# Performance work log

Measured on AMD Instinct MI355X. Metric: run time of the kernel, lower is better.

Reference implementation:

```python
import jax, jax.numpy as jnp
import numpy as np

N, E, D, L, RBF = 20000, 320000, 128, 3, 64
CUTOFF = 5.0
LN_EPS = 1e-5


def setup_inputs() -> dict:
    key = jax.random.key(0)
    ks = jax.random.split(key, 20)
    s = 0.05
    inp = {
        'z': jax.random.normal(ks[0], (N, 64), jnp.float32),
        'pos': jax.random.normal(ks[1], (N, 3), jnp.float32),
        'edge_index': jax.random.randint(ks[2], (2, E), 0, N),
        'in_w': jax.random.normal(ks[3], (64, D), jnp.float32) * s,
        'in_b': jnp.zeros((D,), jnp.float32),
        'filt_w': jax.random.normal(ks[4], (RBF, 3 * D), jnp.float32) * s,
        'filt_b': jnp.zeros((3 * D,), jnp.float32),
        'inter_w1': jax.random.normal(ks[5], (L, D, D), jnp.float32) * s,
        'inter_b1': jnp.zeros((L, D), jnp.float32),
        'inter_w2': jax.random.normal(ks[6], (L, D, 3 * D), jnp.float32) * s,
        'inter_b2': jnp.zeros((L, 3 * D), jnp.float32),
        'mix_mu_w': jax.random.normal(ks[7], (L, D, 2 * D), jnp.float32) * s,
        'mix_w1': jax.random.normal(ks[8], (L, 2 * D, D), jnp.float32) * s,
        'mix_b1': jnp.zeros((L, D), jnp.float32),
        'mix_w2': jax.random.normal(ks[9], (L, D, 3 * D), jnp.float32) * s,
        'mix_b2': jnp.zeros((L, 3 * D), jnp.float32),
        'mu_proj_w': jnp.zeros((D,), jnp.float32),  # nn.init.constant_(0.0) in source
        'ln_g': jnp.ones((D,), jnp.float32),
        'ln_b': jnp.zeros((D,), jnp.float32),
    }
    return inp


def painn_forward(z, pos, in_w, in_b, filt_w, filt_b, inter_w1, inter_b1,
                  inter_w2, inter_b2, mix_mu_w, mix_w1, mix_b1, mix_w2, mix_b2,
                  mu_proj_w, ln_g, ln_b, edge_index):
    idx_i, idx_j = edge_index[0], edge_index[1]
    # edge geometry
    r_ij = pos[idx_j] - pos[idx_i]                               # [E,3]
    d_ij = jnp.maximum(jnp.linalg.norm(r_ij, axis=1, keepdims=True), 1e-8)  # [E,1]
    dir_ij = r_ij / d_ij                                          # [E,3]
    # gaussian smearing
    offset = jnp.linspace(0.0, CUTOFF, RBF).astype(jnp.float32)
    coeff = -0.5 / (offset[1] - offset[0]) ** 2
    phi = jnp.exp(coeff * (d_ij - offset) ** 2)                   # [E,RBF]
    # cosine cutoff
    xc = jnp.clip(d_ij / CUTOFF, 0.0, 1.0)
    fcut = 0.5 * (jnp.cos(jnp.pi * xc) + 1.0) * (xc < 1.0)        # [E,1]
    filters = (phi @ filt_w + filt_b) * fcut                      # [E,3D]
    filters = jnp.clip(jnp.nan_to_num(filters), -5.0, 5.0)
    Wij = filters[:, None, :]                                     # [E,1,3D]

    q = jax.nn.silu(z @ in_w + in_b)[:, None, :]                  # [N,1,D]
    mu = jnp.zeros((N, 3, D), q.dtype)                            # [N,3,D]

    for l in range(L):
        # interaction (edge gather -> gate -> scatter-add)
        x = jax.nn.silu(q @ inter_w1[l] + inter_b1[l]) @ inter_w2[l] + inter_b2[l]  # [N,1,3D]
        xj = x[idx_j] * Wij                                       # [E,1,3D]
        dq, dmuR, dmumu = jnp.split(xj, 3, axis=-1)               # each [E,1,D]
        muj = mu[idx_j]                                           # [E,3,D]
        q = q + jax.ops.segment_sum(dq, idx_i, num_segments=N)
        dmu = dmuR * dir_ij[:, :, None] + dmumu * muj             # [E,3,D]
        mu = mu + jax.ops.segment_sum(dmu, idx_i, num_segments=N)
        # intra-atomic mixing
        mu_mix = mu @ mix_mu_w[l]                                  # [N,3,2D]
        mu_V, mu_W = jnp.split(mu_mix, 2, axis=-1)                 # [N,3,D]
        mu_Vn = jnp.sqrt(jnp.sum(mu_V ** 2, axis=-2, keepdims=True) + 1e-8)  # [N,1,D]
        ctx = jnp.concatenate([q, mu_Vn], axis=-1)                 # [N,1,2D]
        xm = jax.nn.silu(ctx @ mix_w1[l] + mix_b1[l]) @ mix_w2[l] + mix_b2[l]  # [N,1,3D]
        dq_i, dmu_i, dqmu_i = jnp.split(xm, 3, axis=-1)
        q = q + dq_i + dqmu_i * jnp.sum(mu_V * mu_W, axis=1, keepdims=True)
        mu = mu + dmu_i * mu_W

    node_attr = jnp.clip(jnp.nan_to_num(q[:, 0, :]), -5.0, 5.0)   # [N,D]
    mean = jnp.mean(node_attr, axis=-1, keepdims=True)
    var = jnp.var(node_attr, axis=-1, keepdims=True)
    node_attr = (node_attr - mean) * jax.lax.rsqrt(var + LN_EPS) * ln_g + ln_b
    node_attr = jnp.nan_to_num(jnp.tanh(node_attr))

    mu = jnp.nan_to_num(mu)
    mu_node = jax.ops.segment_sum(mu[idx_j], idx_i, num_segments=N)  # [N,3,D]
    mu_node = jnp.clip(jnp.nan_to_num(mu_node), -5.0, 5.0)
    pos_attr = jnp.clip(jnp.nan_to_num(mu_node @ mu_proj_w), -5.0, 5.0)  # [N,3]
    return node_attr, pos_attr


def reference(z, pos, edge_index, in_w, in_b, filt_w, filt_b, inter_w1, inter_b1,
              inter_w2, inter_b2, mix_mu_w, mix_w1, mix_b1, mix_w2, mix_b2,
              mu_proj_w, ln_g, ln_b):
    return painn_forward(z, pos, in_w, in_b, filt_w, filt_b, inter_w1, inter_b1,
                         inter_w2, inter_b2, mix_mu_w, mix_w1, mix_b1, mix_w2,
                         mix_b2, mu_proj_w, ln_g, ln_b, edge_index)
```

## Files before the change

kernel.cpp:

```cpp
#include <hip/hip_runtime.h>
#include <math.h>

#ifndef M_PI
#define M_PI 3.14159265358979323846
#endif

static constexpr int N_NODES = 20000;
static constexpr int N_EDGES = 320000;
static constexpr int NLAYER  = 3;
static constexpr int NB_SCAN = (N_NODES + 255) / 256;
static constexpr int TAB_T   = 1024;

typedef _Float16 f16;
typedef __attribute__((ext_vector_type(2))) _Float16 f16x2;
typedef __attribute__((ext_vector_type(8))) _Float16 f16x8;
typedef __attribute__((ext_vector_type(4))) float f32x4;

__device__ __forceinline__ void storev(float* p, float v) { *p = v; }
__device__ __forceinline__ void storev(f16* p, float v)   { *p = (f16)v; }

__global__ void k_hist(const int* __restrict__ idx_i, int* __restrict__ cnt) {
  int e = blockIdx.x * 256 + threadIdx.x;
  if (e < N_EDGES) atomicAdd(&cnt[idx_i[e]], 1);
}

__global__ void k_scan_blk(const int* __restrict__ cnt, int* __restrict__ incl,
                           int* __restrict__ bsum) {
  __shared__ int buf[256];
  int t = threadIdx.x;
  int i = blockIdx.x * 256 + t;
  int v = (i < N_NODES) ? cnt[i] : 0;
  buf[t] = v;
  __syncthreads();
  #pragma unroll
  for (int off = 1; off < 256; off <<= 1) {
    int x = (t >= off) ? buf[t - off] : 0;
    __syncthreads();
    buf[t] += x;
    __syncthreads();
  }
  if (i < N_NODES) incl[i] = buf[t];
  if (t == 255) bsum[blockIdx.x] = buf[255];
}

__global__ void k_scan_top(int* __restrict__ bsum) {
  __shared__ int buf[128];
  int t = threadIdx.x;
  int v = (t < NB_SCAN) ? bsum[t] : 0;
  buf[t] = v;
  __syncthreads();
  #pragma unroll
  for (int off = 1; off < 128; off <<= 1) {
    int x = (t >= off) ? buf[t - off] : 0;
    __syncthreads();
    buf[t] += x;
    __syncthreads();
  }
  if (t <= NB_SCAN) bsum[t] = buf[t] - v;
}

__global__ void k_scan_add(const int* __restrict__ cnt, const int* __restrict__ incl,
                           const int* __restrict__ bsum, int* __restrict__ rs,
                           int* __restrict__ cur) {
  int i = blockIdx.x * 256 + threadIdx.x;
  if (i < N_NODES) {
    int v = bsum[blockIdx.x] + incl[i] - cnt[i];
    rs[i] = v;
    cur[i] = v;
  }
  if (i == 0) rs[N_NODES] = bsum[NB_SCAN];
}

__global__ void k_fill_geom(const int* __restrict__ idx_all, const float* __restrict__ pos,
                            int* __restrict__ cur, float4* __restrict__ geo,
                            int* __restrict__ jperm) {
  int e = blockIdx.x * 256 + threadIdx.x;
  if (e >= N_EDGES) return;
  int i = idx_all[e];
  int j = idx_all[N_EDGES + e];
  int p = atomicAdd(&cur[i], 1);
  float rx = pos[j*3+0] - pos[i*3+0];
  float ry = pos[j*3+1] - pos[i*3+1];
  float rz = pos[j*3+2] - pos[i*3+2];
  float d = sqrtf(rx*rx + ry*ry + rz*rz);
  d = fmaxf(d, 1e-8f);
  float inv = 1.0f / d;
  geo[p] = make_float4(d, rx*inv, ry*inv, rz*inv);
  jperm[p] = j;
}

struct WJob { const float* src; f16* dst; int kshift; int ld; int col0; int nk; };
struct WJobs { WJob j[16]; };

__global__ __launch_bounds__(256) void k_prep(WJobs jb, const float* __restrict__ filt_w,
                                              const float* __restrict__ filt_b,
                                              f16* __restrict__ tab) {
  if (blockIdx.y < 16) {
    WJob w = jb.j[blockIdx.y];
    int t = blockIdx.x * 256 + threadIdx.x;
    if (t >= w.nk) return;
    int K = 1 << w.kshift;
    int n = t >> w.kshift;
    int k = t & (K - 1);
    w.dst[t] = (f16)w.src[(size_t)k * w.ld + w.col0 + n];
    return;
  }
  if (blockIdx.x >= 128) return;
  const int t = (blockIdx.y - 16) * 128 + blockIdx.x;
  __shared__ float ph[64];
  const int tid = threadIdx.x;
  const float dist = 5.0f * (float)t / (float)(TAB_T - 1);
  const float delta = 5.0f / 63.0f;
  const float coeff = -0.5f / (delta * delta);
  if (tid < 64) {
    float u = dist - delta * (float)tid;
    ph[tid] = expf(coeff * u * u);
  }
  __syncthreads();
  float xc = dist * 0.2f;
  float fc = (xc < 1.0f) ? 0.5f * (cosf((float)M_PI * xc) + 1.0f) : 0.0f;
  for (int n = tid; n < 384; n += 256) {
    float acc = 0.f;
    #pragma unroll
    for (int k = 0; k < 64; ++k) acc += ph[k] * filt_w[k * 384 + n];
    float v = (acc + filt_b[n]) * fc;
    v = fminf(fmaxf(v, -5.0f), 5.0f);
    tab[(size_t)t * 384 + n] = (f16)v;
  }
}

template<int EPI, typename AT, typename CT>
__global__ __launch_bounds__(256) void k_mgemm(
    const AT* __restrict__ A, const f16* __restrict__ Wt,
    const float* __restrict__ bias, CT* __restrict__ C,
    int M, int K, int ldc) {
  __shared__ f16 As[128 * 32];
  __shared__ f16 Bs[128 * 32];
  const int bm = blockIdx.x * 128;
  const int bn = blockIdx.y * 128;
  const int tid = threadIdx.x;
  const int wave = tid >> 6, lane = tid & 63;
  const int wm = (wave & 1) * 64, wn = (wave >> 1) * 64;
  const int lr = lane & 15;
  const int lk = lane >> 4;
  const int srow = tid >> 1;
  const int sc0 = (tid & 1) * 2;
  const int sw = (srow >> 1) & 3;
  f32x4 acc[4][4] = {};
  for (int k0 = 0; k0 < K; k0 += 32) {
    {
      int gm = bm + srow;
      f16x8 c0, c1;
      if (gm < M) {
        if constexpr (sizeof(AT) == 2) {
          const f16* ap = (const f16*)A + (size_t)gm * K + k0 + sc0 * 8;
          c0 = *(const f16x8*)ap;
          c1 = *(const f16x8*)(ap + 8);
        } else {
          const float* ap = (const float*)A + (size_t)gm * K + k0 + sc0 * 8;
          float4 v0 = ((const float4*)ap)[0];
          float4 v1 = ((const float4*)ap)[1];
          float4 v2 = ((const float4*)ap)[2];
          float4 v3 = ((const float4*)ap)[3];
          c0[0]=(f16)v0.x; c0[1]=(f16)v0.y; c0[2]=(f16)v0.z; c0[3]=(f16)v0.w;
          c0[4]=(f16)v1.x; c0[5]=(f16)v1.y; c0[6]=(f16)v1.z; c0[7]=(f16)v1.w;
          c1[0]=(f16)v2.x; c1[1]=(f16)v2.y; c1[2]=(f16)v2.z; c1[3]=(f16)v2.w;
          c1[4]=(f16)v3.x; c1[5]=(f16)v3.y; c1[6]=(f16)v3.z; c1[7]=(f16)v3.w;
        }
      } else {
        #pragma unroll
        for (int u = 0; u < 8; ++u) { c0[u] = (f16)0.f; c1[u] = (f16)0.f; }
      }
      *(f16x8*)&As[srow * 32 + ((sc0 ^ sw) << 3)]       = c0;
      *(f16x8*)&As[srow * 32 + (((sc0 + 1) ^ sw) << 3)] = c1;
    }
    {
      const f16* bp = Wt + (size_t)(bn + srow) * K + k0 + sc0 * 8;
      f16x8 b0 = *(const f16x8*)bp;
      f16x8 b1 = *(const f16x8*)(bp + 8);
      *(f16x8*)&Bs[srow * 32 + ((sc0 ^ sw) << 3)]       = b0;
      *(f16x8*)&Bs[srow * 32 + (((sc0 + 1) ^ sw) << 3)] = b1;
    }
    __syncthreads();
    f16x8 af[4], bf[4];
    #pragma unroll
    for (int mt = 0; mt < 4; ++mt) {
      int r = wm + mt * 16 + lr;
      af[mt] = *(const f16x8*)&As[r * 32 + ((lk ^ ((r >> 1) & 3)) << 3)];
    }
    #pragma unroll
    for (int nt = 0; nt < 4; ++nt) {
      int r = wn + nt * 16 + lr;
      bf[nt] = *(const f16x8*)&Bs[r * 32 + ((lk ^ ((r >> 1) & 3)) << 3)];
    }
    #pragma unroll
    for (int mt = 0; mt < 4; ++mt)
      #pragma unroll
      for (int nt = 0; nt < 4; ++nt)
        acc[mt][nt] = __builtin_amdgcn_mfma_f32_16x16x32_f16(af[mt], bf[nt], acc[mt][nt], 0, 0, 0);
    __syncthreads();
  }
  #pragma unroll
  for (int mt = 0; mt < 4; ++mt) {
    int gm0 = bm + wm + mt * 16 + lk * 4;
    #pragma unroll
    for (int nt = 0; nt < 4; ++nt) {
      int gn = bn + wn + nt * 16 + lr;
      float bv = bias ? bias[gn] : 0.0f;
      #pragma unroll
      for (int rr = 0; rr < 4; ++rr) {
        int gm = gm0 + rr;
        if (gm >= M) continue;
        float v = acc[mt][nt][rr] + bv;
        if (EPI == 1) v = v / (1.0f + expf(-v));
        storev(&C[(size_t)gm * ldc + gn], v);
      }
    }
  }
}

__global__ __launch_bounds__(256) void k_fused_i(
    const float* __restrict__ q, const f16* __restrict__ W1, const float* __restrict__ b1,
    const f16* __restrict__ W2, const float* __restrict__ b2,
    f16* __restrict__ xout, int M) {
  __shared__ f16 As[64 * 32];
  __shared__ f16 Hs[64 * 132];
  const int tid = threadIdx.x;
  const int wave = tid >> 6, lane = tid & 63;
  const int wm = (wave & 1) * 32, wn = (wave >> 1) * 64;
  const int lr = lane & 15, lk = lane >> 4;
  const int srow = tid >> 2, c8 = tid & 3;
  const int sw = (srow >> 1) & 3;
  const int bm = blockIdx.x * 64;
  f32x4 acc[2][4] = {};
  for (int k0 = 0; k0 < 128; k0 += 32) {
    {
      int gm = bm + srow;
      f16x8 c0;
      if (gm < M) {
        const float* ap = q + (size_t)gm * 128 + k0 + c8 * 8;
        float4 v0 = ((const float4*)ap)[0];
        float4 v1 = ((const float4*)ap)[1];
        c0[0]=(f16)v0.x; c0[1]=(f16)v0.y; c0[2]=(f16)v0.z; c0[3]=(f16)v0.w;
        c0[4]=(f16)v1.x; c0[5]=(f16)v1.y; c0[6]=(f16)v1.z; c0[7]=(f16)v1.w;
      } else {
        #pragma unroll
        for (int u = 0; u < 8; ++u) c0[u] = (f16)0.f;
      }
      *(f16x8*)&As[srow * 32 + ((c8 ^ sw) << 3)] = c0;
    }
    __syncthreads();
    f16x8 af[2], bf[4];
    #pragma unroll
    for (int mt = 0; mt < 2; ++mt) {
      int r = wm + mt * 16 + lr;
      af[mt] = *(const f16x8*)&As[r * 32 + ((lk ^ ((r >> 1) & 3)) << 3)];
    }
    #pragma unroll
    for (int nt = 0; nt < 4; ++nt)
      bf[nt] = *(const f16x8*)&W1[(size_t)(wn + nt * 16 + lr) * 128 + k0 + lk * 8];
    #pragma unroll
    for (int mt = 0; mt < 2; ++mt)
      #pragma unroll
      for (int nt = 0; nt < 4; ++nt)
        acc[mt][nt] = __builtin_amdgcn_mfma_f32_16x16x32_f16(af[mt], bf[nt], acc[mt][nt], 0, 0, 0);
    __syncthreads();
  }
  #pragma unroll
  for (int mt = 0; mt < 2; ++mt)
    #pragma unroll
    for (int nt = 0; nt < 4; ++nt) {
      int col = wn + nt * 16 + lr;
      float bv = b1[col];
      #pragma unroll
      for (int rr = 0; rr < 4; ++rr) {
        int row = wm + mt * 16 + lk * 4 + rr;
        float v = acc[mt][nt][rr] + bv;
        v = v / (1.0f + expf(-v));
        Hs[row * 132 + col] = (f16)v;
      }
    }
  __syncthreads();
  #pragma unroll
  for (int cc = 0; cc < 3; ++cc) {
    f32x4 a2[2][4] = {};
    for (int k0 = 0; k0 < 128; k0 += 32) {
      f16x8 af2[2], bf2[4];
      #pragma unroll
      for (int mt = 0; mt < 2; ++mt)
        af2[mt] = *(const f16x8*)&Hs[(wm + mt * 16 + lr) * 132 + k0 + lk * 8];
      #pragma unroll
      for (int nt = 0; nt < 4; ++nt)
        bf2[nt] = *(const f16x8*)&W2[(size_t)(cc * 128 + wn + nt * 16 + lr) * 128 + k0 + lk * 8];
      #pragma unroll
      for (int mt = 0; mt < 2; ++mt)
        #pragma unroll
        for (int nt = 0; nt < 4; ++nt)
          a2[mt][nt] = __builtin_amdgcn_mfma_f32_16x16x32_f16(af2[mt], bf2[nt], a2[mt][nt], 0, 0, 0);
    }
    #pragma unroll
    for (int mt = 0; mt < 2; ++mt)
      #pragma unroll
      for (int nt = 0; nt < 4; ++nt) {
        int gn = cc * 128 + wn + nt * 16 + lr;
        float bv = b2[gn];
        #pragma unroll
        for (int rr = 0; rr < 4; ++rr) {
          int gm = bm + wm + mt * 16 + lk * 4 + rr;
          if (gm >= M) continue;
          xout[(size_t)gm * 384 + gn] = (f16)(a2[mt][nt][rr] + bv);
        }
      }
  }
}

__global__ __launch_bounds__(256) void k_fused_mx(
    float* __restrict__ q, f16* __restrict__ mu,
    const f16* __restrict__ Wmu,
    const f16* __restrict__ W1, const float* __restrict__ b1,
    const f16* __restrict__ W2, const float* __restrict__ b2) {
  __shared__ __align__(16) char pool[50688 + 24576];
  f16* MM  = (f16*)pool;
  f16* As4 = (f16*)(pool + 50688);
  f16* VN  = (f16*)(pool + 50688);
  f16* HS  = (f16*)(pool + 50688 + 8192);

  const int tid = threadIdx.x;
  const int wave = tid >> 6, lane = tid & 63;
  const int lr = lane & 15, lk = lane >> 4;
  const int n0 = blockIdx.x * 32;
  const int r0 = n0 * 3;

  #pragma unroll
  for (int rep = 0; rep < 6; ++rep) {
    int idx = rep * 256 + tid;
    int row = idx >> 4;
    int g   = idx & 15;
    int kb = g >> 2, c8 = g & 3;
    f16x8 v = *(const f16x8*)(mu + (size_t)(r0 + row) * 128 + g * 8);
    *(f16x8*)&As4[((kb * 96 + row) << 5) + (((c8 ^ ((row >> 1) & 3))) << 3)] = v;
  }
  __syncthreads();

  const int wmA = (wave & 1) * 48;
  const int wnA0 = (wave >> 1) * 64;
  #pragma unroll
  for (int half = 0; half < 2; ++half) {
    f32x4 accA[3][4] = {};
    #pragma unroll
    for (int kk = 0; kk < 4; ++kk) {
      f16x8 af[3], bf[4];
      #pragma unroll
      for (int mt = 0; mt < 3; ++mt) {
        int r = wmA + mt * 16 + lr;
        af[mt] = *(const f16x8*)&As4[((kk * 96 + r) << 5) + ((lk ^ ((r >> 1) & 3)) << 3)];
      }
      #pragma unroll
      for (int nt = 0; nt < 4; ++nt)
        bf[nt] = *(const f16x8*)&Wmu[(size_t)(half * 128 + wnA0 + nt * 16 + lr) * 128 + kk * 32 + lk * 8];
      #pragma unroll
      for (int mt = 0; mt < 3; ++mt)
        #pragma unroll
        for (int nt = 0; nt < 4; ++nt)
          accA[mt][nt] = __builtin_amdgcn_mfma_f32_16x16x32_f16(af[mt], bf[nt], accA[mt][nt], 0, 0, 0);
    }
    #pragma unroll
    for (int mt = 0; mt < 3; ++mt)
      #pragma unroll
      for (int nt = 0; nt < 4; ++nt) {
        int col = half * 128 + wnA0 + nt * 16 + lr;
        #pragma unroll
        for (int rr = 0; rr < 4; ++rr) {
          int row = wmA + mt * 16 + lk * 4 + rr;
          MM[row * 264 + col] = (f16)accA[mt][nt][rr];
        }
      }
  }
  __syncthreads();

  #pragma unroll
  for (int rep = 0; rep < 16; ++rep) {
    int idx = rep * 256 + tid;
    int nn = idx >> 7, c = idx & 127;
    float V0 = (float)MM[(nn * 3 + 0) * 264 + c];
    float V1 = (float)MM[(nn * 3 + 1) * 264 + c];
    float V2 = (float)MM[(nn * 3 + 2) * 264 + c];
    float vnv = sqrtf(V0 * V0 + V1 * V1 + V2 * V2 + 1e-8f);
    int kb = c >> 5, c8 = (c >> 3) & 3, ce = c & 7;
    VN[((kb * 32 + nn) << 5) + ((c8 ^ ((nn >> 1) & 3)) << 3) + ce] = (f16)vnv;
  }
  __syncthreads();

  const int wmB = (wave & 1) * 16, wnB = (wave >> 1) * 64;
  f32x4 accB[4] = {};
  #pragma unroll
  for (int kk = 0; kk < 8; ++kk) {
    f16x8 af;
    int row = wmB + lr;
    if (kk < 4) {
      const float* qp_ = q + (size_t)(n0 + row) * 128 + kk * 32 + lk * 8;
      float4 v0 = ((const float4*)qp_)[0];
      float4 v1 = ((const float4*)qp_)[1];
      af[0]=(f16)v0.x; af[1]=(f16)v0.y; af[2]=(f16)v0.z; af[3]=(f16)v0.w;
      af[4]=(f16)v1.x; af[5]=(f16)v1.y; af[6]=(f16)v1.z; af[7]=(f16)v1.w;
    } else {
      af = *(const f16x8*)&VN[(((kk - 4) * 32 + row) << 5) + ((lk ^ ((row >> 1) & 3)) << 3)];
    }
    f16x8 bf[4];
    #pragma unroll
    for (int nt = 0; nt < 4; ++nt)
      bf[nt] = *(const f16x8*)&W1[(size_t)(wnB + nt * 16 + lr) * 256 + kk * 32 + lk * 8];
    #pragma unroll
    for (int nt = 0; nt < 4; ++nt)
      accB[nt] = __builtin_amdgcn_mfma_f32_16x16x32_f16(af, bf[nt], accB[nt], 0, 0, 0);
  }
  #pragma unroll
  for (int nt = 0; nt < 4; ++nt) {
    int col = wnB + nt * 16 + lr;
    float bv = b1[col];
    #pragma unroll
    for (int rr = 0; rr < 4; ++rr) {
      int row = wmB + lk * 4 + rr;
      float v = accB[nt][rr] + bv;
      v = v / (1.0f + expf(-v));
      HS[row * 132 + col] = (f16)v;
    }
  }
  __syncthreads();

  f32x4 accC[3][4] = {};
  #pragma unroll
  for (int cc = 0; cc < 3; ++cc)
    #pragma unroll
    for (int kk = 0; kk < 4; ++kk) {
      f16x8 af = *(const f16x8*)&HS[(wmB + lr) * 132 + kk * 32 + lk * 8];
      f16x8 bf[4];
      #pragma unroll
      for (int nt = 0; nt < 4; ++nt)
        bf[nt] = *(const f16x8*)&W2[(size_t)(cc * 128 + wnB + nt * 16 + lr) * 128 + kk * 32 + lk * 8];
      #pragma unroll
      for (int nt = 0; nt < 4; ++nt)
        accC[cc][nt] = __builtin_amdgcn_mfma_f32_16x16x32_f16(af, bf[nt], accC[cc][nt], 0, 0, 0);
    }
  #pragma unroll
  for (int nt = 0; nt < 4; ++nt) {
    int col = wnB + nt * 16 + lr;
    float b_dq = b2[col], b_dmu = b2[128 + col], b_dqmu = b2[256 + col];
    #pragma unroll
    for (int rr = 0; rr < 4; ++rr) {
      int nn = wmB + lk * 4 + rr;
      int gm = n0 + nn;
      float dq   = accC[0][nt][rr] + b_dq;
      float dmu  = accC[1][nt][rr] + b_dmu;
      float dqmu = accC[2][nt][rr] + b_dqmu;
      float V0 = (float)MM[(nn * 3 + 0) * 264 + col], W0 = (float)MM[(nn * 3 + 0) * 264 + 128 + col];
      float V1 = (float)MM[(nn * 3 + 1) * 264 + col], W1v = (float)MM[(nn * 3 + 1) * 264 + 128 + col];
      float V2 = (float)MM[(nn * 3 + 2) * 264 + col], W2v = (float)MM[(nn * 3 + 2) * 264 + 128 + col];
      float svw = V0 * W0 + V1 * W1v + V2 * W2v;
      size_t qi = (size_t)gm * 128 + col;
      q[qi] += dq + dqmu * svw;
      f16* mr = mu + (size_t)gm * 384;
      mr[col]       = (f16)((float)mr[col]       + dmu * W0);
      mr[128 + col] = (f16)((float)mr[128 + col] + dmu * W1v);
      mr[256 + col] = (f16)((float)mr[256 + col] + dmu * W2v);
    }
  }
}

template<bool HASMU>
__global__ __launch_bounds__(256) void k_edge_msg(
    const int* __restrict__ rs, const int* __restrict__ jperm,
    const f16* __restrict__ x, const f16* __restrict__ tab,
    const float4* __restrict__ geo, const f16* __restrict__ mu_in,
    float* __restrict__ q, f16* __restrict__ mu_out) {
  const int wid  = threadIdx.x >> 6;
  const int lane = threadIdx.x & 63;
  const int i = blockIdx.x * 4 + wid;
  if (i >= N_NODES) return;
  const int d0 = lane * 2;
  const float scale = (float)(TAB_T - 1) / 5.0f;
  float aqx = 0.f, aqy = 0.f;
  float a0x = 0.f, a0y = 0.f, a1x = 0.f, a1y = 0.f, a2x = 0.f, a2y = 0.f;
  const int s = rs[i], e = rs[i + 1];

  for (int p = s; p < e; ++p) {
    int j = jperm[p];
    float4 g = geo[p];
    float u = fminf(g.x, 5.0f) * scale;
    int t0 = min((int)u, TAB_T - 2);
    float fr = u - (float)t0, fo = 1.0f - fr;
    const f16* ta = tab + (size_t)t0 * 384;
    const f16* xj = x + (size_t)j * 384;
    f16x2 ta0 = *(const f16x2*)(ta + d0);
    f16x2 ta1 = *(const f16x2*)(ta + 128 + d0);
    f16x2 tb0 = *(const f16x2*)(ta + 384 + d0);
    f16x2 tb1 = *(const f16x2*)(ta + 512 + d0);
    f16x2 xv0 = *(const f16x2*)(xj + d0);
    f16x2 xv1 = *(const f16x2*)(xj + 128 + d0);
    float W0x = fo * (float)ta0[0] + fr * (float)tb0[0];
    float W0y = fo * (float)ta0[1] + fr * (float)tb0[1];
    float W1x = fo * (float)ta1[0] + fr * (float)tb1[0];
    float W1y = fo * (float)ta1[1] + fr * (float)tb1[1];
    float m1x = (float)xv1[0] * W1x, m1y = (float)xv1[1] * W1y;
    aqx = fmaf((float)xv0[0], W0x, aqx);
    aqy = fmaf((float)xv0[1], W0y, aqy);
    if constexpr (HASMU) {
      f16x2 ta2 = *(const f16x2*)(ta + 256 + d0);
      f16x2 tb2 = *(const f16x2*)(ta + 640 + d0);
      f16x2 xv2 = *(const f16x2*)(xj + 256 + d0);
      const f16* mj = mu_in + (size_t)j * 384;
      f16x2 mv0 = *(const f16x2*)(mj + d0);
      f16x2 mv1 = *(const f16x2*)(mj + 128 + d0);
      f16x2 mv2 = *(const f16x2*)(mj + 256 + d0);
      float W2x = fo * (float)ta2[0] + fr * (float)tb2[0];
      float W2y = fo * (float)ta2[1] + fr * (float)tb2[1];
      float m2x = (float)xv2[0] * W2x, m2y = (float)xv2[1] * W2y;
      a0x += m1x * g.y + m2x * (float)mv0[0];
      a0y += m1y * g.y + m2y * (float)mv0[1];
      a1x += m1x * g.z + m2x * (float)mv1[0];
      a1y += m1y * g.z + m2y * (float)mv1[1];
      a2x += m1x * g.w + m2x * (float)mv2[0];
      a2y += m1y * g.w + m2y * (float)mv2[1];
    } else {
      a0x += m1x * g.y; a0y += m1y * g.y;
      a1x += m1x * g.z; a1y += m1y * g.z;
      a2x += m1x * g.w; a2y += m1y * g.w;
    }
  }

  float* qp = q + (size_t)i * 128 + d0;
  float2 qv = *(float2*)qp;
  qv.x += aqx; qv.y += aqy;
  *(float2*)qp = qv;
  f16* mout = mu_out + (size_t)i * 384;
  f16x2 o0, o1, o2;
  if constexpr (HASMU) {
    const f16* min_ = mu_in + (size_t)i * 384;
    f16x2 i0 = *(const f16x2*)(min_ + d0);
    f16x2 i1 = *(const f16x2*)(min_ + 128 + d0);
    f16x2 i2 = *(const f16x2*)(min_ + 256 + d0);
    o0[0] = (f16)((float)i0[0] + a0x); o0[1] = (f16)((float)i0[1] + a0y);
    o1[0] = (f16)((float)i1[0] + a1x); o1[1] = (f16)((float)i1[1] + a1y);
    o2[0] = (f16)((float)i2[0] + a2x); o2[1] = (f16)((float)i2[1] + a2y);
  } else {
    o0[0] = (f16)a0x; o0[1] = (f16)a0y;
    o1[0] = (f16)a1x; o1[1] = (f16)a1y;
    o2[0] = (f16)a2x; o2[1] = (f16)a2y;
  }
  *(f16x2*)(mout + d0)       = o0;
  *(f16x2*)(mout + 128 + d0) = o1;
  *(f16x2*)(mout + 256 + d0) = o2;
}

__global__ __launch_bounds__(256) void k_outputs(
    const int* __restrict__ rs, const int* __restrict__ jperm,
    const f16* __restrict__ mu, const float* __restrict__ w, float* __restrict__ pos_out,
    const float* __restrict__ q, const float* __restrict__ g_, const float* __restrict__ b_,
    float* __restrict__ out_node) {
  const int wid  = threadIdx.x >> 6;
  const int lane = threadIdx.x & 63;
  const int i = blockIdx.x * 4 + wid;
  if (i >= N_NODES) return;
  const int d0 = lane * 2;
  if (blockIdx.y == 1) {
    float2 v = *(const float2*)(q + (size_t)i * 128 + d0);
    float v0 = fminf(fmaxf(v.x, -5.f), 5.f);
    float v1 = fminf(fmaxf(v.y, -5.f), 5.f);
    float s = v0 + v1, s2 = v0 * v0 + v1 * v1;
    #pragma unroll
    for (int off = 32; off > 0; off >>= 1) {
      s  += __shfl_down(s,  off, 64);
      s2 += __shfl_down(s2, off, 64);
    }
    s  = __shfl(s,  0, 64);
    s2 = __shfl(s2, 0, 64);
    float mean = s * (1.0f / 128.0f);
    float var  = s2 * (1.0f / 128.0f) - mean * mean;
    float r = rsqrtf(var + 1e-5f);
    out_node[(size_t)i * 128 + d0]     = tanhf((v0 - mean) * r * g_[d0]     + b_[d0]);
    out_node[(size_t)i * 128 + d0 + 1] = tanhf((v1 - mean) * r * g_[d0 + 1] + b_[d0 + 1]);
    return;
  }
  float a0x = 0.f, a0y = 0.f, a1x = 0.f, a1y = 0.f, a2x = 0.f, a2y = 0.f;
  const int s = rs[i], e = rs[i + 1];
  int p = s;
  for (; p + 2 <= e; p += 2) {
    int jA = jperm[p], jB = jperm[p + 1];
    const f16* mA = mu + (size_t)jA * 384;
    const f16* mB = mu + (size_t)jB * 384;
    f16x2 A0 = *(const f16x2*)(mA + d0);
    f16x2 A1 = *(const f16x2*)(mA + 128 + d0);
    f16x2 A2 = *(const f16x2*)(mA + 256 + d0);
    f16x2 B0 = *(const f16x2*)(mB + d0);
    f16x2 B1 = *(const f16x2*)(mB + 128 + d0);
    f16x2 B2 = *(const f16x2*)(mB + 256 + d0);
    a0x += (float)A0[0] + (float)B0[0]; a0y += (float)A0[1] + (float)B0[1];
    a1x += (float)A1[0] + (float)B1[0]; a1y += (float)A1[1] + (float)B1[1];
    a2x += (float)A2[0] + (float)B2[0]; a2y += (float)A2[1] + (float)B2[1];
  }
  for (; p < e; ++p) {
    int j = jperm[p];
    const f16* mj = mu + (size_t)j * 384;
    f16x2 A0 = *(const f16x2*)(mj + d0);
    f16x2 A1 = *(const f16x2*)(mj + 128 + d0);
    f16x2 A2 = *(const f16x2*)(mj + 256 + d0);
    a0x += (float)A0[0]; a0y += (float)A0[1];
    a1x += (float)A1[0]; a1y += (float)A1[1];
    a2x += (float)A2[0]; a2y += (float)A2[1];
  }
  float wx = w[d0], wy = w[d0 + 1];
  float s0 = fminf(fmaxf(a0x, -5.f), 5.f) * wx + fminf(fmaxf(a0y, -5.f), 5.f) * wy;
  float s1 = fminf(fmaxf(a1x, -5.f), 5.f) * wx + fminf(fmaxf(a1y, -5.f), 5.f) * wy;
  float s2 = fminf(fmaxf(a2x, -5.f), 5.f) * wx + fminf(fmaxf(a2y, -5.f), 5.f) * wy;
  #pragma unroll
  for (int off = 32; off > 0; off >>= 1) {
    s0 += __shfl_down(s0, off, 64);
    s1 += __shfl_down(s1, off, 64);
    s2 += __shfl_down(s2, off, 64);
  }
  if (lane == 0) {
    pos_out[(size_t)i * 3 + 0] = fminf(fmaxf(s0, -5.f), 5.f);
    pos_out[(size_t)i * 3 + 1] = fminf(fmaxf(s1, -5.f), 5.f);
    pos_out[(size_t)i * 3 + 2] = fminf(fmaxf(s2, -5.f), 5.f);
  }
}

extern "C" void kernel_launch(void* const* d_in, const int* in_sizes, int n_in,
                              void* d_out, int out_size, void* d_ws, size_t ws_size,
                              hipStream_t stream) {
  const float* z         = (const float*)d_in[0];
  const float* pos       = (const float*)d_in[1];
  const int*   edge_idx  = (const int*)d_in[2];
  const float* in_w      = (const float*)d_in[3];
  const float* in_b      = (const float*)d_in[4];
  const float* filt_w    = (const float*)d_in[5];
  const float* filt_b    = (const float*)d_in[6];
  const float* inter_w1  = (const float*)d_in[7];
  const float* inter_b1  = (const float*)d_in[8];
  const float* inter_w2  = (const float*)d_in[9];
  const float* inter_b2  = (const float*)d_in[10];
  const float* mix_mu_w  = (const float*)d_in[11];
  const float* mix_w1    = (const float*)d_in[12];
  const float* mix_b1    = (const float*)d_in[13];
  const float* mix_w2    = (const float*)d_in[14];
  const float* mix_b2    = (const float*)d_in[15];
  const float* mu_proj_w = (const float*)d_in[16];
  const float* ln_g      = (const float*)d_in[17];
  const float* ln_b      = (const float*)d_in[18];

  char* base = (char*)d_ws;
  size_t off = 0;
  auto alloc = [&](size_t bytes) -> char* {
    char* p = base + off;
    off += (bytes + 255) & ~(size_t)255;
    return p;
  };
  float*  q     = (float*)alloc((size_t)N_NODES * 128 * 4);
  f16*    x16   = (f16*)alloc((size_t)N_NODES * 384 * 2);
  f16*    mu_a  = (f16*)alloc((size_t)N_NODES * 384 * 2);
  f16*    mu_b  = (f16*)alloc((size_t)N_NODES * 384 * 2);
  float4* geo   = (float4*)alloc((size_t)N_EDGES * 16);
  int*    cnt   = (int*)alloc((size_t)N_NODES * 4);
  int*    incl  = (int*)alloc((size_t)N_NODES * 4);
  int*    bsum  = (int*)alloc(128 * 4);
  int*    rs    = (int*)alloc((size_t)(N_NODES + 1) * 4);
  int*    cur   = (int*)alloc((size_t)N_NODES * 4);
  int*    jperm = (int*)alloc((size_t)N_EDGES * 4);
  f16*    tab   = (f16*)alloc((size_t)TAB_T * 384 * 2);
  f16* wt_in = (f16*)alloc((size_t)128 * 64 * 2);
  f16* wt_i1 = (f16*)alloc((size_t)3 * 128 * 128 * 2);
  f16* wt_i2 = (f16*)alloc((size_t)3 * 384 * 128 * 2);
  f16* wt_mu = (f16*)alloc((size_t)3 * 256 * 128 * 2);
  f16* wt_x1 = (f16*)alloc((size_t)3 * 128 * 256 * 2);
  f16* wt_x2 = (f16*)alloc((size_t)3 * 384 * 128 * 2);
  if (off > ws_size) return;

  float* out_node = (float*)d_out;
  float* out_pos  = (float*)d_out + (size_t)N_NODES * 128;

  {
    WJobs jb;
    int ji = 0;
    jb.j[ji++] = {in_w, wt_in, 6, 128, 0, 128 * 64};
    for (int l = 0; l < 3; ++l)
      jb.j[ji++] = {inter_w1 + (size_t)l*128*128, wt_i1 + (size_t)l*128*128, 7, 128, 0, 128*128};
    for (int l = 0; l < 3; ++l)
      jb.j[ji++] = {inter_w2 + (size_t)l*128*384, wt_i2 + (size_t)l*384*128, 7, 384, 0, 384*128};
    for (int l = 0; l < 3; ++l)
      jb.j[ji++] = {mix_mu_w + (size_t)l*128*256, wt_mu + (size_t)l*256*128, 7, 256, 0, 256*128};
    for (int l = 0; l < 3; ++l)
      jb.j[ji++] = {mix_w1 + (size_t)l*256*128, wt_x1 + (size_t)l*128*256, 8, 128, 0, 128*256};
    for (int l = 0; l < 3; ++l)
      jb.j[ji++] = {mix_w2 + (size_t)l*128*384, wt_x2 + (size_t)l*384*128, 7, 384, 0, 384*128};
    dim3 g(192, 24);
    k_prep<<<g, 256, 0, stream>>>(jb, filt_w, filt_b, tab);
  }

  hipMemsetAsync(cnt, 0, (size_t)N_NODES * 4, stream);
  k_hist<<<N_EDGES / 256, 256, 0, stream>>>(edge_idx, cnt);
  k_scan_blk<<<NB_SCAN, 256, 0, stream>>>(cnt, incl, bsum);
  k_scan_top<<<1, 128, 0, stream>>>(bsum);
  k_scan_add<<<NB_SCAN, 256, 0, stream>>>(cnt, incl, bsum, rs, cur);
  k_fill_geom<<<N_EDGES / 256, 256, 0, stream>>>(edge_idx, pos, cur, geo, jperm);

  dim3 ge((N_NODES + 127) / 128, 1);
  k_mgemm<1, float, float><<<ge, 256, 0, stream>>>(z, wt_in, in_b, q, N_NODES, 64, 128);

  f16* mu_cur = mu_a;
  f16* mu_nxt = mu_b;
  const int gn4 = (N_NODES + 3) / 4;
  const int gf  = (N_NODES + 63) / 64;
  const int gmx = N_NODES / 32;
  for (int l = 0; l < NLAYER; ++l) {
    k_fused_i<<<gf, 256, 0, stream>>>(q, wt_i1 + (size_t)l*128*128, inter_b1 + (size_t)l*128,
                                      wt_i2 + (size_t)l*384*128, inter_b2 + (size_t)l*384,
                                      x16, N_NODES);
    if (l == 0)
      k_edge_msg<false><<<gn4, 256, 0, stream>>>(rs, jperm, x16, tab, geo, mu_cur, q, mu_nxt);
    else
      k_edge_msg<true><<<gn4, 256, 0, stream>>>(rs, jperm, x16, tab, geo, mu_cur, q, mu_nxt);
    { f16* t = mu_cur; mu_cur = mu_nxt; mu_nxt = t; }
    k_fused_mx<<<gmx, 256, 0, stream>>>(q, mu_cur, wt_mu + (size_t)l*256*128,
                                        wt_x1 + (size_t)l*128*256, mix_b1 + (size_t)l*128,
                                        wt_x2 + (size_t)l*384*128, mix_b2 + (size_t)l*384);
  }

  dim3 go(gn4, 2);
  k_outputs<<<go, 256, 0, stream>>>(rs, jperm, mu_cur, mu_proj_w, out_pos,
                                    q, ln_g, ln_b, out_node);
}
```

Measured before the change: 587.3 us.

## Fuse interaction MLP into embedding and previous mix kernels; skip zero-weight gather

```diff
diff --git a/kernel.cpp b/kernel.cpp
--- a/kernel.cpp
+++ b/kernel.cpp
@@ -15,9 +15,6 @@
 typedef __attribute__((ext_vector_type(2))) _Float16 f16x2;
 typedef __attribute__((ext_vector_type(8))) _Float16 f16x8;
 typedef __attribute__((ext_vector_type(4))) float f32x4;
-
-__device__ __forceinline__ void storev(float* p, float v) { *p = v; }
-__device__ __forceinline__ void storev(f16* p, float v)   { *p = (f16)v; }
 
 __global__ void k_hist(const int* __restrict__ idx_i, int* __restrict__ cnt) {
   int e = blockIdx.x * 256 + threadIdx.x;
@@ -129,201 +126,125 @@
   }
 }
 
-template<int EPI, typename AT, typename CT>
-__global__ __launch_bounds__(256) void k_mgemm(
-    const AT* __restrict__ A, const f16* __restrict__ Wt,
-    const float* __restrict__ bias, CT* __restrict__ C,
-    int M, int K, int ldc) {
-  __shared__ f16 As[128 * 32];
-  __shared__ f16 Bs[128 * 32];
-  const int bm = blockIdx.x * 128;
-  const int bn = blockIdx.y * 128;
+__global__ __launch_bounds__(256) void k_embed_i(
+    const float* __restrict__ z, const f16* __restrict__ Win, const float* __restrict__ bin,
+    const f16* __restrict__ Wi1, const float* __restrict__ bi1,
+    const f16* __restrict__ Wi2, const float* __restrict__ bi2,
+    float* __restrict__ q, f16* __restrict__ xout) {
+  __shared__ __align__(16) char pool[16896];
+  f16* QS  = (f16*)pool;
+  f16* H2S = (f16*)(pool + 8448);
   const int tid = threadIdx.x;
   const int wave = tid >> 6, lane = tid & 63;
-  const int wm = (wave & 1) * 64, wn = (wave >> 1) * 64;
-  const int lr = lane & 15;
-  const int lk = lane >> 4;
-  const int srow = tid >> 1;
-  const int sc0 = (tid & 1) * 2;
-  const int sw = (srow >> 1) & 3;
-  f32x4 acc[4][4] = {};
-  for (int k0 = 0; k0 < K; k0 += 32) {
-    {
-      int gm = bm + srow;
-      f16x8 c0, c1;
-      if (gm < M) {
-        if constexpr (sizeof(AT) == 2) {
-          const f16* ap = (const f16*)A + (size_t)gm * K + k0 + sc0 * 8;
-          c0 = *(const f16x8*)ap;
-          c1 = *(const f16x8*)(ap + 8);
-        } else {
-          const float* ap = (const float*)A + (size_t)gm * K + k0 + sc0 * 8;
-          float4 v0 = ((const float4*)ap)[0];
-          float4 v1 = ((const float4*)ap)[1];
-          float4 v2 = ((const float4*)ap)[2];
-          float4 v3 = ((const float4*)ap)[3];
-          c0[0]=(f16)v0.x; c0[1]=(f16)v0.y; c0[2]=(f16)v0.z; c0[3]=(f16)v0.w;
-          c0[4]=(f16)v1.x; c0[5]=(f16)v1.y; c0[6]=(f16)v1.z; c0[7]=(f16)v1.w;
-          c1[0]=(f16)v2.x; c1[1]=(f16)v2.y; c1[2]=(f16)v2.z; c1[3]=(f16)v2.w;
-          c1[4]=(f16)v3.x; c1[5]=(f16)v3.y; c1[6]=(f16)v3.z; c1[7]=(f16)v3.w;
-        }
-      } else {
-        #pragma unroll
-        for (int u = 0; u < 8; ++u) { c0[u] = (f16)0.f; c1[u] = (f16)0.f; }
+  const int lr = lane & 15, lk = lane >> 4;
+  const int wmB = (wave & 1) * 16, wnB = (wave >> 1) * 64;
+  const int n0 = blockIdx.x * 32;
+
+  f32x4 accP[4] = {};
+  #pragma unroll
+  for (int kk = 0; kk < 2; ++kk) {
+    const float* zp = z + (size_t)(n0 + wmB + lr) * 64 + kk * 32 + lk * 8;
+    float4 v0 = ((const float4*)zp)[0];
+    float4 v1 = ((const float4*)zp)[1];
+    f16x8 af;
+    af[0]=(f16)v0.x; af[1]=(f16)v0.y; af[2]=(f16)v0.z; af[3]=(f16)v0.w;
+    af[4]=(f16)v1.x; af[5]=(f16)v1.y; af[6]=(f16)v1.z; af[7]=(f16)v1.w;
+    f16x8 bf[4];
+    #pragma unroll
+    for (int nt = 0; nt < 4; ++nt)
+      bf[nt] = *(const f16x8*)&Win[(size_t)(wnB + nt * 16 + lr) * 64 + kk * 32 + lk * 8];
+    #pragma unroll
+    for (int nt = 0; nt < 4; ++nt)
+      accP[nt] = __builtin_amdgcn_mfma_f32_16x16x32_f16(af, bf[nt], accP[nt], 0, 0, 0);
+  }
+  #pragma unroll
+  for (int nt = 0; nt < 4; ++nt) {
+    int col = wnB + nt * 16 + lr;
+    float bv = bin[col];
+    #pragma unroll
+    for (int rr = 0; rr < 4; ++rr) {
+      int row = wmB + lk * 4 + rr;
+      float v = accP[nt][rr] + bv;
+      v = v / (1.0f + expf(-v));
+      q[(size_t)(n0 + row) * 128 + col] = v;
+      QS[row * 132 + col] = (f16)v;
+    }
+  }
+  __syncthreads();
+
+  f32x4 accD[4] = {};
+  #pragma unroll
+  for (int kk = 0; kk < 4; ++kk) {
+    f16x8 af = *(const f16x8*)&QS[(wmB + lr) * 132 + kk * 32 + lk * 8];
+    f16x8 bf[4];
+    #pragma unroll
+    for (int nt = 0; nt < 4; ++nt)
+      bf[nt] = *(const f16x8*)&Wi1[(size_t)(wnB + nt * 16 + lr) * 128 + kk * 32 + lk * 8];
+    #pragma unroll
+    for (int nt = 0; nt < 4; ++nt)
+      accD[nt] = __builtin_amdgcn_mfma_f32_16x16x32_f16(af, bf[nt], accD[nt], 0, 0, 0);
+  }
+  #pragma unroll
+  for (int nt = 0; nt < 4; ++nt) {
+    int col = wnB + nt * 16 + lr;
+    float bv = bi1[col];
+    #pragma unroll
+    for (int rr = 0; rr < 4; ++rr) {
+      int row = wmB + lk * 4 + rr;
+      float v = accD[nt][rr] + bv;
+      v = v / (1.0f + expf(-v));
+      H2S[row * 132 + col] = (f16)v;
+    }
+  }
+  __syncthreads();
+
+  #pragma unroll
+  for (int cc = 0; cc < 3; ++cc) {
+    f32x4 accE[4] = {};
+    #pragma unroll
+    for (int kk = 0; kk < 4; ++kk) {
+      f16x8 af = *(const f16x8*)&H2S[(wmB + lr) * 132 + kk * 32 + lk * 8];
+      f16x8 bf[4];
+      #pragma unroll
+      for (int nt = 0; nt < 4; ++nt)
+        bf[nt] = *(const f16x8*)&Wi2[(size_t)(cc * 128 + wnB + nt * 16 + lr) * 128 + kk * 32 + lk * 8];
+      #pragma unroll
+      for (int nt = 0; nt < 4; ++nt)
+        accE[nt] = __builtin_amdgcn_mfma_f32_16x16x32_f16(af, bf[nt], accE[nt], 0, 0, 0);
+    }
+    #pragma unroll
+    for (int nt = 0; nt < 4; ++nt) {
+      int gn = cc * 128 + wnB + nt * 16 + lr;
+      float bv = bi2[gn];
+      #pragma unroll
+      for (int rr = 0; rr < 4; ++rr) {
+        int gm = n0 + wmB + lk * 4 + rr;
+        xout[(size_t)gm * 384 + gn] = (f16)(accE[nt][rr] + bv);
       }
-      *(f16x8*)&As[srow * 32 + ((sc0 ^ sw) << 3)]       = c0;
-      *(f16x8*)&As[srow * 32 + (((sc0 + 1) ^ sw) << 3)] = c1;
-    }
-    {
-      const f16* bp = Wt + (size_t)(bn + srow) * K + k0 + sc0 * 8;
-      f16x8 b0 = *(const f16x8*)bp;
-      f16x8 b1 = *(const f16x8*)(bp + 8);
-      *(f16x8*)&Bs[srow * 32 + ((sc0 ^ sw) << 3)]       = b0;
-      *(f16x8*)&Bs[srow * 32 + (((sc0 + 1) ^ sw) << 3)] = b1;
-    }
-    __syncthreads();
-    f16x8 af[4], bf[4];
-    #pragma unroll
-    for (int mt = 0; mt < 4; ++mt) {
-      int r = wm + mt * 16 + lr;
-      af[mt] = *(const f16x8*)&As[r * 32 + ((lk ^ ((r >> 1) & 3)) << 3)];
-    }
-    #pragma unroll
-    for (int nt = 0; nt < 4; ++nt) {
-      int r = wn + nt * 16 + lr;
-      bf[nt] = *(const f16x8*)&Bs[r * 32 + ((lk ^ ((r >> 1) & 3)) << 3)];
-    }
-    #pragma unroll
-    for (int mt = 0; mt < 4; ++mt)
-      #pragma unroll
-      for (int nt = 0; nt < 4; ++nt)
-        acc[mt][nt] = __builtin_amdgcn_mfma_f32_16x16x32_f16(af[mt], bf[nt], acc[mt][nt], 0, 0, 0);
-    __syncthreads();
-  }
-  #pragma unroll
-  for (int mt = 0; mt < 4; ++mt) {
-    int gm0 = bm + wm + mt * 16 + lk * 4;
-    #pragma unroll
-    for (int nt = 0; nt < 4; ++nt) {
-      int gn = bn + wn + nt * 16 + lr;
-      float bv = bias ? bias[gn] : 0.0f;
-      #pragma unroll
-      for (int rr = 0; rr < 4; ++rr) {
-        int gm = gm0 + rr;
-        if (gm >= M) continue;
-        float v = acc[mt][nt][rr] + bv;
-        if (EPI == 1) v = v / (1.0f + expf(-v));
-        storev(&C[(size_t)gm * ldc + gn], v);
-      }
-    }
-  }
-}
-
-__global__ __launch_bounds__(256) void k_fused_i(
-    const float* __restrict__ q, const f16* __restrict__ W1, const float* __restrict__ b1,
-    const f16* __restrict__ W2, const float* __restrict__ b2,
-    f16* __restrict__ xout, int M) {
-  __shared__ f16 As[64 * 32];
-  __shared__ f16 Hs[64 * 132];
-  const int tid = threadIdx.x;
-  const int wave = tid >> 6, lane = tid & 63;
-  const int wm = (wave & 1) * 32, wn = (wave >> 1) * 64;
-  const int lr = lane & 15, lk = lane >> 4;
-  const int srow = tid >> 2, c8 = tid & 3;
-  const int sw = (srow >> 1) & 3;
-  const int bm = blockIdx.x * 64;
-  f32x4 acc[2][4] = {};
-  for (int k0 = 0; k0 < 128; k0 += 32) {
-    {
-      int gm = bm + srow;
-      f16x8 c0;
-      if (gm < M) {
-        const float* ap = q + (size_t)gm * 128 + k0 + c8 * 8;
-        float4 v0 = ((const float4*)ap)[0];
-        float4 v1 = ((const float4*)ap)[1];
-        c0[0]=(f16)v0.x; c0[1]=(f16)v0.y; c0[2]=(f16)v0.z; c0[3]=(f16)v0.w;
-        c0[4]=(f16)v1.x; c0[5]=(f16)v1.y; c0[6]=(f16)v1.z; c0[7]=(f16)v1.w;
-      } else {
-        #pragma unroll
-        for (int u = 0; u < 8; ++u) c0[u] = (f16)0.f;
-      }
-      *(f16x8*)&As[srow * 32 + ((c8 ^ sw) << 3)] = c0;
-    }
-    __syncthreads();
-    f16x8 af[2], bf[4];
-    #pragma unroll
-    for (int mt = 0; mt < 2; ++mt) {
-      int r = wm + mt * 16 + lr;
-      af[mt] = *(const f16x8*)&As[r * 32 + ((lk ^ ((r >> 1) & 3)) << 3)];
-    }
-    #pragma unroll
-    for (int nt = 0; nt < 4; ++nt)
-      bf[nt] = *(const f16x8*)&W1[(size_t)(wn + nt * 16 + lr) * 128 + k0 + lk * 8];
-    #pragma unroll
-    for (int mt = 0; mt < 2; ++mt)
-      #pragma unroll
-      for (int nt = 0; nt < 4; ++nt)
-        acc[mt][nt] = __builtin_amdgcn_mfma_f32_16x16x32_f16(af[mt], bf[nt], acc[mt][nt], 0, 0, 0);
-    __syncthreads();
-  }
-  #pragma unroll
-  for (int mt = 0; mt < 2; ++mt)
-    #pragma unroll
-    for (int nt = 0; nt < 4; ++nt) {
-      int col = wn + nt * 16 + lr;
-      float bv = b1[col];
-      #pragma unroll
-      for (int rr = 0; rr < 4; ++rr) {
-        int row = wm + mt * 16 + lk * 4 + rr;
-        float v = acc[mt][nt][rr] + bv;
-        v = v / (1.0f + expf(-v));
-        Hs[row * 132 + col] = (f16)v;
-      }
-    }
-  __syncthreads();
-  #pragma unroll
-  for (int cc = 0; cc < 3; ++cc) {
-    f32x4 a2[2][4] = {};
-    for (int k0 = 0; k0 < 128; k0 += 32) {
-      f16x8 af2[2], bf2[4];
-      #pragma unroll
-      for (int mt = 0; mt < 2; ++mt)
-        af2[mt] = *(const f16x8*)&Hs[(wm + mt * 16 + lr) * 132 + k0 + lk * 8];
-      #pragma unroll
-      for (int nt = 0; nt < 4; ++nt)
-        bf2[nt] = *(const f16x8*)&W2[(size_t)(cc * 128 + wn + nt * 16 + lr) * 128 + k0 + lk * 8];
-      #pragma unroll
-      for (int mt = 0; mt < 2; ++mt)
-        #pragma unroll
-        for (int nt = 0; nt < 4; ++nt)
-          a2[mt][nt] = __builtin_amdgcn_mfma_f32_16x16x32_f16(af2[mt], bf2[nt], a2[mt][nt], 0, 0, 0);
-    }
-    #pragma unroll
-    for (int mt = 0; mt < 2; ++mt)
-      #pragma unroll
-      for (int nt = 0; nt < 4; ++nt) {
-        int gn = cc * 128 + wn + nt * 16 + lr;
-        float bv = b2[gn];
-        #pragma unroll
-        for (int rr = 0; rr < 4; ++rr) {
-          int gm = bm + wm + mt * 16 + lk * 4 + rr;
-          if (gm >= M) continue;
-          xout[(size_t)gm * 384 + gn] = (f16)(a2[mt][nt][rr] + bv);
-        }
-      }
-  }
-}
-
-__global__ __launch_bounds__(256) void k_fused_mx(
+    }
+  }
+}
+
+template<int MODE>
+__global__ __launch_bounds__(256) void k_mix(
     float* __restrict__ q, f16* __restrict__ mu,
     const f16* __restrict__ Wmu,
     const f16* __restrict__ W1, const float* __restrict__ b1,
-    const f16* __restrict__ W2, const float* __restrict__ b2) {
-  __shared__ __align__(16) char pool[50688 + 24576];
-  f16* MM  = (f16*)pool;
-  f16* As4 = (f16*)(pool + 50688);
-  f16* VN  = (f16*)(pool + 50688);
-  f16* HS  = (f16*)(pool + 50688 + 8192);
+    const f16* __restrict__ W2, const float* __restrict__ b2,
+    const f16* __restrict__ Wi1, const float* __restrict__ bi1,
+    const f16* __restrict__ Wi2, const float* __restrict__ bi2,
+    f16* __restrict__ xout,
+    const float* __restrict__ ln_g, const float* __restrict__ ln_b,
+    float* __restrict__ out_node) {
+  __shared__ __align__(16) char pool[50688 + 25344];
+  f16*   MM  = (f16*)pool;
+  char*  scr = pool + 50688;
+  f16*   As4 = (f16*)scr;
+  f16*   VN  = (f16*)scr;
+  f16*   HS  = (f16*)(scr + 8448);
+  f16*   QS  = (f16*)(scr + 16896);
+  f16*   H2S = (f16*)scr;
+  float* QSf = (float*)scr;
 
   const int tid = threadIdx.x;
   const int wave = tid >> 6, lane = tid & 63;
@@ -338,7 +259,7 @@
     int g   = idx & 15;
     int kb = g >> 2, c8 = g & 3;
     f16x8 v = *(const f16x8*)(mu + (size_t)(r0 + row) * 128 + g * 8);
-    *(f16x8*)&As4[((kb * 96 + row) << 5) + (((c8 ^ ((row >> 1) & 3))) << 3)] = v;
+    *(f16x8*)&As4[((kb * 96 + row) << 5) + ((c8 ^ ((row >> 1) & 3)) << 3)] = v;
   }
   __syncthreads();
 
@@ -442,6 +363,8 @@
       for (int nt = 0; nt < 4; ++nt)
         accC[cc][nt] = __builtin_amdgcn_mfma_f32_16x16x32_f16(af, bf[nt], accC[cc][nt], 0, 0, 0);
     }
+  __syncthreads();
+
   #pragma unroll
   for (int nt = 0; nt < 4; ++nt) {
     int col = wnB + nt * 16 + lr;
@@ -458,11 +381,95 @@
       float V2 = (float)MM[(nn * 3 + 2) * 264 + col], W2v = (float)MM[(nn * 3 + 2) * 264 + 128 + col];
       float svw = V0 * W0 + V1 * W1v + V2 * W2v;
       size_t qi = (size_t)gm * 128 + col;
-      q[qi] += dq + dqmu * svw;
+      float qnew = q[qi] + dq + dqmu * svw;
+      if constexpr (MODE == 0) {
+        q[qi] = qnew;
+        QS[nn * 132 + col] = (f16)qnew;
+      } else {
+        QSf[nn * 132 + col] = qnew;
+      }
       f16* mr = mu + (size_t)gm * 384;
       mr[col]       = (f16)((float)mr[col]       + dmu * W0);
       mr[128 + col] = (f16)((float)mr[128 + col] + dmu * W1v);
       mr[256 + col] = (f16)((float)mr[256 + col] + dmu * W2v);
+    }
+  }
+  __syncthreads();
+
+  if constexpr (MODE == 0) {
+    f32x4 accD[4] = {};
+    #pragma unroll
+    for (int kk = 0; kk < 4; ++kk) {
+      f16x8 af = *(const f16x8*)&QS[(wmB + lr) * 132 + kk * 32 + lk * 8];
+      f16x8 bf[4];
+      #pragma unroll
+      for (int nt = 0; nt < 4; ++nt)
+        bf[nt] = *(const f16x8*)&Wi1[(size_t)(wnB + nt * 16 + lr) * 128 + kk * 32 + lk * 8];
+      #pragma unroll
+      for (int nt = 0; nt < 4; ++nt)
+        accD[nt] = __builtin_amdgcn_mfma_f32_16x16x32_f16(af, bf[nt], accD[nt], 0, 0, 0);
+    }
+    #pragma unroll
+    for (int nt = 0; nt < 4; ++nt) {
+      int col = wnB + nt * 16 + lr;
+      float bv = bi1[col];
+      #pragma unroll
+      for (int rr = 0; rr < 4; ++rr) {
+        int row = wmB + lk * 4 + rr;
+        float v = accD[nt][rr] + bv;
+        v = v / (1.0f + expf(-v));
+        H2S[row * 132 + col] = (f16)v;
+      }
+    }
+    __syncthreads();
+    #pragma unroll
+    for (int cc = 0; cc < 3; ++cc) {
+      f32x4 accE[4] = {};
+      #pragma unroll
+      for (int kk = 0; kk < 4; ++kk) {
+        f16x8 af = *(const f16x8*)&H2S[(wmB + lr) * 132 + kk * 32 + lk * 8];
+        f16x8 bf[4];
+        #pragma unroll
+        for (int nt = 0; nt < 4; ++nt)
+          bf[nt] = *(const f16x8*)&Wi2[(size_t)(cc * 128 + wnB + nt * 16 + lr) * 128 + kk * 32 + lk * 8];
+        #pragma unroll
+        for (int nt = 0; nt < 4; ++nt)
+          accE[nt] = __builtin_amdgcn_mfma_f32_16x16x32_f16(af, bf[nt], accE[nt], 0, 0, 0);
+      }
+      #pragma unroll
+      for (int nt = 0; nt < 4; ++nt) {
+        int gn = cc * 128 + wnB + nt * 16 + lr;
+        float bv = bi2[gn];
+        #pragma unroll
+        for (int rr = 0; rr < 4; ++rr) {
+          int gm = n0 + wmB + lk * 4 + rr;
+          xout[(size_t)gm * 384 + gn] = (f16)(accE[nt][rr] + bv);
+        }
+      }
+    }
+  } else {
+    const int d0 = lane * 2;
+    #pragma unroll
+    for (int rr2 = 0; rr2 < 8; ++rr2) {
+      int nn = wave * 8 + rr2;
+      float v0 = QSf[nn * 132 + d0];
+      float v1 = QSf[nn * 132 + d0 + 1];
+      v0 = fminf(fmaxf(v0, -5.f), 5.f);
+      v1 = fminf(fmaxf(v1, -5.f), 5.f);
+      float s = v0 + v1, s2 = v0 * v0 + v1 * v1;
+      #pragma unroll
+      for (int off = 32; off > 0; off >>= 1) {
+        s  += __shfl_down(s,  off, 64);
+        s2 += __shfl_down(s2, off, 64);
+      }
+      s  = __shfl(s,  0, 64);
+      s2 = __shfl(s2, 0, 64);
+      float mean = s * (1.0f / 128.0f);
+      float var  = s2 * (1.0f / 128.0f) - mean * mean;
+      float r = rsqrtf(var + 1e-5f);
+      size_t o = (size_t)(n0 + nn) * 128 + d0;
+      out_node[o]     = tanhf((v0 - mean) * r * ln_g[d0]     + ln_b[d0]);
+      out_node[o + 1] = tanhf((v1 - mean) * r * ln_g[d0 + 1] + ln_b[d0 + 1]);
     }
   }
 }
@@ -552,63 +559,29 @@
   *(f16x2*)(mout + 256 + d0) = o2;
 }
 
-__global__ __launch_bounds__(256) void k_outputs(
+__global__ __launch_bounds__(256) void k_posattr(
     const int* __restrict__ rs, const int* __restrict__ jperm,
-    const f16* __restrict__ mu, const float* __restrict__ w, float* __restrict__ pos_out,
-    const float* __restrict__ q, const float* __restrict__ g_, const float* __restrict__ b_,
-    float* __restrict__ out_node) {
+    const f16* __restrict__ mu, const float* __restrict__ w, float* __restrict__ pos_out) {
   const int wid  = threadIdx.x >> 6;
   const int lane = threadIdx.x & 63;
   const int i = blockIdx.x * 4 + wid;
   if (i >= N_NODES) return;
   const int d0 = lane * 2;
-  if (blockIdx.y == 1) {
-    float2 v = *(const float2*)(q + (size_t)i * 128 + d0);
-    float v0 = fminf(fmaxf(v.x, -5.f), 5.f);
-    float v1 = fminf(fmaxf(v.y, -5.f), 5.f);
-    float s = v0 + v1, s2 = v0 * v0 + v1 * v1;
-    #pragma unroll
-    for (int off = 32; off > 0; off >>= 1) {
-      s  += __shfl_down(s,  off, 64);
-      s2 += __shfl_down(s2, off, 64);
-    }
-    s  = __shfl(s,  0, 64);
-    s2 = __shfl(s2, 0, 64);
-    float mean = s * (1.0f / 128.0f);
-    float var  = s2 * (1.0f / 128.0f) - mean * mean;
-    float r = rsqrtf(var + 1e-5f);
-    out_node[(size_t)i * 128 + d0]     = tanhf((v0 - mean) * r * g_[d0]     + b_[d0]);
-    out_node[(size_t)i * 128 + d0 + 1] = tanhf((v1 - mean) * r * g_[d0 + 1] + b_[d0 + 1]);
-    return;
-  }
   float a0x = 0.f, a0y = 0.f, a1x = 0.f, a1y = 0.f, a2x = 0.f, a2y = 0.f;
-  const int s = rs[i], e = rs[i + 1];
-  int p = s;
-  for (; p + 2 <= e; p += 2) {
-    int jA = jperm[p], jB = jperm[p + 1];
-    const f16* mA = mu + (size_t)jA * 384;
-    const f16* mB = mu + (size_t)jB * 384;
-    f16x2 A0 = *(const f16x2*)(mA + d0);
-    f16x2 A1 = *(const f16x2*)(mA + 128 + d0);
-    f16x2 A2 = *(const f16x2*)(mA + 256 + d0);
-    f16x2 B0 = *(const f16x2*)(mB + d0);
-    f16x2 B1 = *(const f16x2*)(mB + 128 + d0);
-    f16x2 B2 = *(const f16x2*)(mB + 256 + d0);
-    a0x += (float)A0[0] + (float)B0[0]; a0y += (float)A0[1] + (float)B0[1];
-    a1x += (float)A1[0] + (float)B1[0]; a1y += (float)A1[1] + (float)B1[1];
-    a2x += (float)A2[0] + (float)B2[0]; a2y += (float)A2[1] + (float)B2[1];
-  }
-  for (; p < e; ++p) {
-    int j = jperm[p];
-    const f16* mj = mu + (size_t)j * 384;
-    f16x2 A0 = *(const f16x2*)(mj + d0);
-    f16x2 A1 = *(const f16x2*)(mj + 128 + d0);
-    f16x2 A2 = *(const f16x2*)(mj + 256 + d0);
-    a0x += (float)A0[0]; a0y += (float)A0[1];
-    a1x += (float)A1[0]; a1y += (float)A1[1];
-    a2x += (float)A2[0]; a2y += (float)A2[1];
-  }
   float wx = w[d0], wy = w[d0 + 1];
+  if (wx != 0.0f || wy != 0.0f) {
+    const int s = rs[i], e = rs[i + 1];
+    for (int p = s; p < e; ++p) {
+      int j = jperm[p];
+      const f16* mj = mu + (size_t)j * 384;
+      f16x2 A0 = *(const f16x2*)(mj + d0);
+      f16x2 A1 = *(const f16x2*)(mj + 128 + d0);
+      f16x2 A2 = *(const f16x2*)(mj + 256 + d0);
+      a0x += (float)A0[0]; a0y += (float)A0[1];
+      a1x += (float)A1[0]; a1y += (float)A1[1];
+      a2x += (float)A2[0]; a2y += (float)A2[1];
+    }
+  }
   float s0 = fminf(fmaxf(a0x, -5.f), 5.f) * wx + fminf(fmaxf(a0y, -5.f), 5.f) * wy;
   float s1 = fminf(fmaxf(a1x, -5.f), 5.f) * wx + fminf(fmaxf(a1y, -5.f), 5.f) * wy;
   float s2 = fminf(fmaxf(a2x, -5.f), 5.f) * wx + fminf(fmaxf(a2y, -5.f), 5.f) * wy;
@@ -703,29 +676,34 @@
   k_scan_add<<<NB_SCAN, 256, 0, stream>>>(cnt, incl, bsum, rs, cur);
   k_fill_geom<<<N_EDGES / 256, 256, 0, stream>>>(edge_idx, pos, cur, geo, jperm);
 
-  dim3 ge((N_NODES + 127) / 128, 1);
-  k_mgemm<1, float, float><<<ge, 256, 0, stream>>>(z, wt_in, in_b, q, N_NODES, 64, 128);
+  const int gmx = N_NODES / 32;
+  const int gn4 = (N_NODES + 3) / 4;
+  k_embed_i<<<gmx, 256, 0, stream>>>(z, wt_in, in_b,
+                                     wt_i1, inter_b1, wt_i2, inter_b2, q, x16);
 
   f16* mu_cur = mu_a;
   f16* mu_nxt = mu_b;
-  const int gn4 = (N_NODES + 3) / 4;
-  const int gf  = (N_NODES + 63) / 64;
-  const int gmx = N_NODES / 32;
   for (int l = 0; l < NLAYER; ++l) {
-    k_fused_i<<<gf, 256, 0, stream>>>(q, wt_i1 + (size_t)l*128*128, inter_b1 + (size_t)l*128,
-                                      wt_i2 + (size_t)l*384*128, inter_b2 + (size_t)l*384,
-                                      x16, N_NODES);
     if (l == 0)
       k_edge_msg<false><<<gn4, 256, 0, stream>>>(rs, jperm, x16, tab, geo, mu_cur, q, mu_nxt);
     else
       k_edge_msg<true><<<gn4, 256, 0, stream>>>(rs, jperm, x16, tab, geo, mu_cur, q, mu_nxt);
     { f16* t = mu_cur; mu_cur = mu_nxt; mu_nxt = t; }
-    k_fused_mx<<<gmx, 256, 0, stream>>>(q, mu_cur, wt_mu + (size_t)l*256*128,
+    if (l < NLAYER - 1) {
+      k_mix<0><<<gmx, 256, 0, stream>>>(q, mu_cur, wt_mu + (size_t)l*256*128,
                                         wt_x1 + (size_t)l*128*256, mix_b1 + (size_t)l*128,
-                                        wt_x2 + (size_t)l*384*128, mix_b2 + (size_t)l*384);
-  }
-
-  dim3 go(gn4, 2);
-  k_outputs<<<go, 256, 0, stream>>>(rs, jperm, mu_cur, mu_proj_w, out_pos,
-                                    q, ln_g, ln_b, out_node);
-}
+                                        wt_x2 + (size_t)l*384*128, mix_b2 + (size_t)l*384,
+                                        wt_i1 + (size_t)(l+1)*128*128, inter_b1 + (size_t)(l+1)*128,
+                                        wt_i2 + (size_t)(l+1)*384*128, inter_b2 + (size_t)(l+1)*384,
+                                        x16, nullptr, nullptr, nullptr);
+    } else {
+      k_mix<1><<<gmx, 256, 0, stream>>>(q, mu_cur, wt_mu + (size_t)l*256*128,
+                                        wt_x1 + (size_t)l*128*256, mix_b1 + (size_t)l*128,
+                                        wt_x2 + (size_t)l*384*128, mix_b2 + (size_t)l*384,
+                                        nullptr, nullptr, nullptr, nullptr, nullptr,
+                                        ln_g, ln_b, out_node);
+    }
+  }
+
+  k_posattr<<<gn4, 256, 0, stream>>>(rs, jperm, mu_cur, mu_proj_w, out_pos);
+}
```

New measurement: 546.3 us (median of 2 runs). 1.08x faster.
